# Kernel tuning notes

Hardware: AMD Instinct MI355X
Metric: run time of the kernel (lower is better)

The kernel has to match this reference:

```python
import jax, jax.numpy as jnp
import numpy as np

IN, H, L = 512, 1024, 2
N, T = 64, 256


def setup_inputs() -> dict:
    key = jax.random.key(0)
    ks = jax.random.split(key, 1 + 4 * L)
    x = jax.random.normal(ks[0], (N, T, IN), dtype=jnp.float32)
    inp = {"x": x}
    for l in range(L):
        d_in = IN if l == 0 else H
        s_x = 1.0 / np.sqrt(d_in)
        s_h = 1.0 / np.sqrt(H)
        # concatenated gate order: [i, f, g, o]
        inp[f"Wx{l}"] = jax.random.normal(ks[1 + 4 * l], (4 * H, d_in), dtype=jnp.float32) * s_x
        inp[f"Wh{l}"] = jax.random.normal(ks[2 + 4 * l], (4 * H, H), dtype=jnp.float32) * s_h
        inp[f"b{l}"] = jax.random.normal(ks[3 + 4 * l], (4 * H,), dtype=jnp.float32) * 0.1
        # peephole weights for [i, f, o] (original inits these to zero; randomized here)
        inp[f"Wc{l}"] = jax.random.normal(ks[4 + 4 * l], (3, H), dtype=jnp.float32) * 0.1
    return inp


def _lstm_forward(x, params):
    # params: list of (Wx [4H,d_in], Wh [4H,H], b [4H], Wc [3,H]) per layer
    n = x.shape[0]
    h0 = jnp.zeros((L, n, H), dtype=x.dtype)
    c0 = jnp.zeros((L, n, H), dtype=x.dtype)

    def step(carry, x_t):
        hs, cs = carry
        new_h, new_c = [], []
        inp_t = x_t
        for l, (Wx, Wh, b, Wc) in enumerate(params):
            h, c = hs[l], cs[l]
            gates = inp_t @ Wx.T + h @ Wh.T + b  # [n, 4H]
            gi, gf, gg, go = jnp.split(gates, 4, axis=-1)
            i = jax.nn.sigmoid(gi + Wc[0] * c)
            f = jax.nn.sigmoid(gf + Wc[1] * c)  # computed but unused (faithful to source)
            g = jnp.tanh(gg)
            o = jax.nn.sigmoid(go + Wc[2] * c)
            ct = g * c + i * g          # faithful: forget gate not applied
            ht = o * jnp.tanh(c)        # faithful: uses OLD cell state
            new_h.append(ht)
            new_c.append(ct)
            inp_t = ht  # dropout p=0 -> identity
        hs = jnp.stack(new_h)
        cs = jnp.stack(new_c)
        return (hs, cs), new_h[-1]

    (hs, cs), outs = jax.lax.scan(step, (h0, c0), jnp.swapaxes(x, 0, 1))
    out = jnp.swapaxes(outs, 0, 1)  # [N, T, H]
    return out, (hs[-1], cs[-1])


def reference(x, Wx0, Wh0, b0, Wc0, Wx1, Wh1, b1, Wc1):
    params = [(Wx0, Wh0, b0, Wc0), (Wx1, Wh1, b1, Wc1)]
    return _lstm_forward(x, params)
```

## Files before the change

### kernel.cpp

```cpp
#include <hip/hip_runtime.h>
#include <stdint.h>


#define T_STEPS 256
#define HDIM    1024
#define NB      64
#define INDIM   512
#define NWG     256
#define TPB     256
#define PRING   8

typedef _Float16 f16;
typedef __attribute__((ext_vector_type(8))) _Float16 f16x8;
typedef __attribute__((ext_vector_type(4))) float    f32x4;

#define CNT_OFF 0
#define XB_OFF  81920
#define H0_OFF  16859136
#define H1_OFF  50544640
#define C0_OFF  84230144
#define C1_OFF  84492288
#define P0_OFF  84754432
#define P1_OFF  91045888

__device__ __forceinline__ float sigm(float x)     { return 1.0f / (1.0f + __expf(-x)); }
__device__ __forceinline__ float tanhfast(float x) { float e = __expf(2.0f * x); return 1.0f - 2.0f / (e + 1.0f); }

__device__ __forceinline__ void arrive(int* c) {
  __hip_atomic_fetch_add(c, 1, __ATOMIC_RELAXED, __HIP_MEMORY_SCOPE_AGENT);
}
__device__ __forceinline__ void wait_ge(int* c, int v) {
  while (__hip_atomic_load(c, __ATOMIC_RELAXED, __HIP_MEMORY_SCOPE_AGENT) < v)
    __builtin_amdgcn_s_sleep(1);
  __atomic_signal_fence(__ATOMIC_ACQUIRE);
}
__device__ __forceinline__ void wait_flag(int* f, int tgt) {
  while (__hip_atomic_load(f, __ATOMIC_RELAXED, __HIP_MEMORY_SCOPE_AGENT) < tgt)
    __builtin_amdgcn_s_sleep(1);
}
__device__ __forceinline__ void sti(int* p, int v) {
  __hip_atomic_store(p, v, __ATOMIC_RELAXED, __HIP_MEMORY_SCOPE_AGENT);
}
__device__ __forceinline__ void st2h(f16* p, float a, float b) {
  union { f16 h[2]; uint32_t u; } cc; cc.h[0] = (f16)a; cc.h[1] = (f16)b;
  __hip_atomic_store((uint32_t*)p, cc.u, __ATOMIC_RELAXED, __HIP_MEMORY_SCOPE_AGENT);
}
__device__ __forceinline__ void st8a(void* p, unsigned long long v) {
  __hip_atomic_store((unsigned long long*)p, v, __ATOMIC_RELAXED, __HIP_MEMORY_SCOPE_AGENT);
}
__device__ __forceinline__ unsigned long long ld8(const float* p) {
  return __hip_atomic_load((const unsigned long long*)p, __ATOMIC_RELAXED, __HIP_MEMORY_SCOPE_AGENT);
}

template<int K>
__device__ __forceinline__ void gemm48_lds(const f16* __restrict__ Aw,
                                           const f16* wl, int lr, int wv, int quad,
                                           f32x4 (&acc)[4][3]) {
  constexpr int NIT = K / 128;
  const f16* a0 = Aw + (size_t)(lr +  0) * K;
  const f16* a1 = Aw + (size_t)(lr + 16) * K;
  const f16* a2 = Aw + (size_t)(lr + 32) * K;
  const f16* a3 = Aw + (size_t)(lr + 48) * K;
  f16x8 A0[NIT], A1[NIT], A2[NIT], A3[NIT];
#pragma unroll
  for (int it = 0; it < NIT; ++it) {
    const int kk = it * 32;
    A0[it] = *(const f16x8*)(a0 + kk);
    A1[it] = *(const f16x8*)(a1 + kk);
    A2[it] = *(const f16x8*)(a2 + kk);
    A3[it] = *(const f16x8*)(a3 + kk);
  }
  const f16* b0r = wl + (size_t)(lr +  0) * K;
  const f16* b1r = wl + (size_t)(lr + 16) * K;
  const f16* b2r = wl + (size_t)(lr + 32) * K;
  const int s  = lr & 7;
  const int cb = wv * (K / 32);
#pragma unroll
  for (int it = 0; it < NIT; ++it) {
    const int ch = ((cb + it * 4 + quad) ^ s) << 3;
    f16x8 B0 = *(const f16x8*)(b0r + ch);
    f16x8 B1 = *(const f16x8*)(b1r + ch);
    f16x8 B2 = *(const f16x8*)(b2r + ch);
    acc[0][0] = __builtin_amdgcn_mfma_f32_16x16x32_f16(A0[it], B0, acc[0][0], 0, 0, 0);
    acc[0][1] = __builtin_amdgcn_mfma_f32_16x16x32_f16(A0[it], B1, acc[0][1], 0, 0, 0);
    acc[0][2] = __builtin_amdgcn_mfma_f32_16x16x32_f16(A0[it], B2, acc[0][2], 0, 0, 0);
    acc[1][0] = __builtin_amdgcn_mfma_f32_16x16x32_f16(A1[it], B0, acc[1][0], 0, 0, 0);
    acc[1][1] = __builtin_amdgcn_mfma_f32_16x16x32_f16(A1[it], B1, acc[1][1], 0, 0, 0);
    acc[1][2] = __builtin_amdgcn_mfma_f32_16x16x32_f16(A1[it], B2, acc[1][2], 0, 0, 0);
    acc[2][0] = __builtin_amdgcn_mfma_f32_16x16x32_f16(A2[it], B0, acc[2][0], 0, 0, 0);
    acc[2][1] = __builtin_amdgcn_mfma_f32_16x16x32_f16(A2[it], B1, acc[2][1], 0, 0, 0);
    acc[2][2] = __builtin_amdgcn_mfma_f32_16x16x32_f16(A2[it], B2, acc[2][2], 0, 0, 0);
    acc[3][0] = __builtin_amdgcn_mfma_f32_16x16x32_f16(A3[it], B0, acc[3][0], 0, 0, 0);
    acc[3][1] = __builtin_amdgcn_mfma_f32_16x16x32_f16(A3[it], B1, acc[3][1], 0, 0, 0);
    acc[3][2] = __builtin_amdgcn_mfma_f32_16x16x32_f16(A3[it], B2, acc[3][2], 0, 0, 0);
  }
}

__global__ __launch_bounds__(TPB, 1) void lstm_pers(
    const float* __restrict__ x,
    const float* __restrict__ Wx0, const float* __restrict__ Wh0,
    const float* __restrict__ b0,  const float* __restrict__ Wc0,
    const float* __restrict__ Wx1, const float* __restrict__ Wh1,
    const float* __restrict__ b1,  const float* __restrict__ Wc1,
    float* __restrict__ out, char* __restrict__ ws)
{
  int* cbase = (int*)(ws + CNT_OFF);
  int* proCnt = cbase;
  auto FLG = [&](int g, int i) { return cbase + 16 + ((g * 64 + i) << 4); };

  f16* XB   = (f16*)(ws + XB_OFF);
  f16* H0   = (f16*)(ws + H0_OFF);
  f16* H1   = (f16*)(ws + H1_OFF);
  float* C0 = (float*)(ws + C0_OFF);
  float* C1 = (float*)(ws + C1_OFF);
  float* P0b = (float*)(ws + P0_OFF);
  float* P1b = (float*)(ws + P1_OFF);

  __shared__ float lds[4][64][52];
  __shared__ f16 wlds[48 * 1024];

  const int tid  = threadIdx.x;
  const int wg   = blockIdx.x;
  const int gtid = wg * TPB + tid;
  const int GSZ  = NWG * TPB;

  const int grp  = wg >> 6;
  const int ug   = wg & 63;
  const int lane = tid & 63;
  const int wv   = tid >> 6;
  const int quad = lane >> 4;
  const int lr   = lane & 15;

  const float* Wsrc; int K;
  switch (grp) {
    case 0:  Wsrc = Wx0; K = 512;  break;
    case 1:  Wsrc = Wh0; K = 1024; break;
    case 2:  Wsrc = Wx1; K = 1024; break;
    default: Wsrc = Wh1; K = 1024; break;
  }
  const int Kq = K >> 2;

  {
    const int rsh = (K == 512) ? 6 : 7;
    const int cpr = 1 << rsh;
    for (int c = tid; c < 48 * cpr; c += TPB) {
      const int row = c >> rsh, ch = c & (cpr - 1);
      const int gate = row >> 4, j = row & 15;
      const int R = ug * 16 + j + (gate == 1 ? 2048 : (gate == 2 ? 3072 : 0));
      const float* src = Wsrc + (size_t)R * K + (ch << 3);
      f32x4 f0 = *(const f32x4*)src;
      f32x4 f1 = *(const f32x4*)(src + 4);
      f16x8 h8;
      h8[0]=(f16)f0[0]; h8[1]=(f16)f0[1]; h8[2]=(f16)f0[2]; h8[3]=(f16)f0[3];
      h8[4]=(f16)f1[0]; h8[5]=(f16)f1[1]; h8[6]=(f16)f1[2]; h8[7]=(f16)f1[3];
      const int chs = ch ^ (row & 7);
      *(f16x8*)(wlds + (size_t)row * K + (chs << 3)) = h8;
    }
  }
  for (int idx = gtid; idx < T_STEPS * NB * 256; idx += GSZ) {
    int t = idx >> 14, n = (idx >> 8) & 63, i2 = (idx & 255) << 1;
    const float* src = x + (size_t)n * (T_STEPS * INDIM) + (size_t)t * INDIM + i2;
    st2h(&XB[(size_t)idx << 1], src[0], src[1]);
  }

  __builtin_amdgcn_s_waitcnt(0);
  __syncthreads();
  if (tid == 0) { arrive(proCnt); wait_ge(proCnt, NWG); }
  __syncthreads();

  const float* bb = (grp == 1) ? b0 : b1;
  const float* wc = (grp == 1) ? Wc0 : Wc1;
  float* cst = (grp == 1) ? C0 : C1;

  const int m_e = tid >> 2, j0 = (tid & 3) << 2;

  for (int t = 0; t < T_STEPS; ++t) {
    if (tid < 64) {
      if (grp == 0)      { if (t >= PRING) wait_flag(FLG(1, tid), t - PRING + 1); }
      else if (grp == 1) { wait_flag(FLG(0, tid), t + 1); if (t) wait_flag(FLG(1, tid), t); }
      else if (grp == 2) { wait_flag(FLG(1, tid), t + 1); if (t >= PRING) wait_flag(FLG(3, tid), t - PRING + 1); }
      else               { wait_flag(FLG(2, tid), t + 1); if (t) wait_flag(FLG(3, tid), t); }
    }
    __atomic_signal_fence(__ATOMIC_ACQUIRE);
    __syncthreads();

    const f16* Abase;
    if (grp == 0)      Abase = XB + (size_t)t * NB * INDIM;
    else if (grp == 1) Abase = H0 + (size_t)t * NB * HDIM;
    else if (grp == 2) Abase = H0 + (size_t)(t + 1) * NB * HDIM;
    else               Abase = H1 + (size_t)t * NB * HDIM;

    unsigned long long pr0, pr1, pr2, pr3, pr4, pr5;
    if (grp & 1) {
      const float* Pb = (grp == 1 ? P0b : P1b) + (size_t)(t & (PRING - 1)) * NB * 3072;
      const float* pbase = Pb + (size_t)m_e * 3072 + ug * 48 + j0;
      pr0 = ld8(pbase);      pr1 = ld8(pbase + 2);
      pr2 = ld8(pbase + 16); pr3 = ld8(pbase + 18);
      pr4 = ld8(pbase + 32); pr5 = ld8(pbase + 34);
    }

    f32x4 acc[4][3];
#pragma unroll
    for (int mt = 0; mt < 4; ++mt)
#pragma unroll
      for (int nt = 0; nt < 3; ++nt)
        acc[mt][nt] = (f32x4){0.f, 0.f, 0.f, 0.f};

    const f16* Aw = Abase + wv * Kq + quad * 8;
    if (grp == 0) gemm48_lds<512>(Aw, wlds, lr, wv, quad, acc);
    else          gemm48_lds<1024>(Aw, wlds, lr, wv, quad, acc);

#pragma unroll
    for (int mt = 0; mt < 4; ++mt)
#pragma unroll
      for (int nt = 0; nt < 3; ++nt)
#pragma unroll
        for (int r = 0; r < 4; ++r)
          lds[wv][mt * 16 + quad * 4 + r][nt * 16 + lr] = acc[mt][nt][r];
    __syncthreads();

    if ((grp & 1) == 0) {
      float* Pb = (grp == 0 ? P0b : P1b) + (size_t)(t & (PRING - 1)) * NB * 3072;
#pragma unroll
      for (int r = 0; r < 6; ++r) {
        const int s  = r * 256 + tid;
        const int m  = s / 24, cp = s - m * 24;
        const int c0 = cp << 1;
        float v0 = lds[0][m][c0]     + lds[1][m][c0]     + lds[2][m][c0]     + lds[3][m][c0];
        float v1 = lds[0][m][c0 + 1] + lds[1][m][c0 + 1] + lds[2][m][c0 + 1] + lds[3][m][c0 + 1];
        union { float f[2]; unsigned long long u; } pp; pp.f[0] = v0; pp.f[1] = v1;
        st8a(Pb + (size_t)m * 3072 + ug * 48 + c0, pp.u);
      }
    } else {
      union { unsigned long long u; float f[2]; } q0, q1, q2, q3, q4, q5;
      q0.u = pr0; q1.u = pr1; q2.u = pr2; q3.u = pr3; q4.u = pr4; q5.u = pr5;
      f32x4 vi = (f32x4){0.f, 0.f, 0.f, 0.f};
      f32x4 vg = vi, vo = vi;
#pragma unroll
      for (int w = 0; w < 4; ++w) {
        vi += *(const f32x4*)&lds[w][m_e][j0];
        vg += *(const f32x4*)&lds[w][m_e][16 + j0];
        vo += *(const f32x4*)&lds[w][m_e][32 + j0];
      }
      const float pif[4] = {q0.f[0], q0.f[1], q1.f[0], q1.f[1]};
      const float pgf[4] = {q2.f[0], q2.f[1], q3.f[0], q3.f[1]};
      const float pof[4] = {q4.f[0], q4.f[1], q5.f[0], q5.f[1]};
      f16* Hdst = (grp == 1 ? H0 : H1) + (size_t)(t + 1) * NB * HDIM;
      const int u0 = ug * 16 + j0;
      float* crow = cst + (size_t)m_e * HDIM + u0;
      f32x4 c4  = *(const f32x4*)crow;
      f32x4 b_i = *(const f32x4*)(bb + u0);
      f32x4 b_g = *(const f32x4*)(bb + 2048 + u0);
      f32x4 b_o = *(const f32x4*)(bb + 3072 + u0);
      f32x4 wci = *(const f32x4*)(wc + u0);
      f32x4 wco = *(const f32x4*)(wc + 2048 + u0);
      f32x4 hv, cn;
#pragma unroll
      for (int k = 0; k < 4; ++k) {
        float gi = vi[k] + pif[k] + b_i[k];
        float gg = vg[k] + pgf[k] + b_g[k];
        float go = vo[k] + pof[k] + b_o[k];
        float cold = c4[k];
        float iv = sigm(gi + wci[k] * cold);
        float gv = tanhfast(gg);
        float ov = sigm(go + wco[k] * cold);
        cn[k] = gv * (cold + iv);
        hv[k] = ov * tanhfast(cold);
      }
      *(f32x4*)crow = cn;
      union { f16 h[4]; unsigned long long u; } hh;
      hh.h[0]=(f16)hv[0]; hh.h[1]=(f16)hv[1]; hh.h[2]=(f16)hv[2]; hh.h[3]=(f16)hv[3];
      st8a(&Hdst[(size_t)m_e * HDIM + u0], hh.u);
      if (grp == 3) {
        *(f32x4*)&out[(size_t)m_e * (T_STEPS * HDIM) + (size_t)t * HDIM + u0] = hv;
        if (t == T_STEPS - 1) {
          *(f32x4*)&out[(size_t)NB * T_STEPS * HDIM + (size_t)m_e * HDIM + u0] = hv;
          *(f32x4*)&out[(size_t)NB * T_STEPS * HDIM + NB * HDIM + (size_t)m_e * HDIM + u0] = cn;
        }
      }
    }

    __builtin_amdgcn_s_waitcnt(0);
    __syncthreads();
    if (tid == 0) sti(FLG(grp, ug), t + 1);
  }
}

extern "C" void kernel_launch(void* const* d_in, const int* in_sizes, int n_in,
                              void* d_out, int out_size, void* d_ws, size_t ws_size,
                              hipStream_t stream) {
  const float* x   = (const float*)d_in[0];
  const float* Wx0 = (const float*)d_in[1];
  const float* Wh0 = (const float*)d_in[2];
  const float* b0  = (const float*)d_in[3];
  const float* Wc0 = (const float*)d_in[4];
  const float* Wx1 = (const float*)d_in[5];
  const float* Wh1 = (const float*)d_in[6];
  const float* b1  = (const float*)d_in[7];
  const float* Wc1 = (const float*)d_in[8];
  char* ws = (char*)d_ws;

  hipMemsetAsync(ws + CNT_OFF, 0, 81920, stream);
  hipMemsetAsync(ws + H0_OFF, 0, NB * HDIM * 2, stream);
  hipMemsetAsync(ws + H1_OFF, 0, NB * HDIM * 2, stream);
  hipMemsetAsync(ws + C0_OFF, 0, 2 * NB * HDIM * 4, stream);

  hipLaunchKernelGGL(lstm_pers, dim3(NWG), dim3(TPB), 0, stream,
                     x, Wx0, Wh0, b0, Wc0, Wx1, Wh1, b1, Wc1,
                     (float*)d_out, ws);
}
```

Before: 2.259 ms.

## Per-wave flag waits, packed flags, hoisted bias loads, output stores after signal

Replaces the step-start barrier, where 64 threads polled every flag before a block-wide __syncthreads, with per-wave waits. Each wave polls only the producer flags covering the 16 units whose rows it consumes, so it can start its GEMM as soon as its own inputs are ready. Flags are packed contiguously instead of padded 64 bytes apart. Bias and peephole weights are loaded once before the time loop, the cell-state load is issued early, and the global output store is moved after the flag publish so it stays off the critical path. The risks are flag false sharing, and whether dropping the barrier keeps correct visibility across waves, for example of the P buffer data.

```diff
diff --git a/kernel.cpp b/kernel.cpp
--- a/kernel.cpp
+++ b/kernel.cpp
@@ -33,10 +33,6 @@
   while (__hip_atomic_load(c, __ATOMIC_RELAXED, __HIP_MEMORY_SCOPE_AGENT) < v)
     __builtin_amdgcn_s_sleep(1);
   __atomic_signal_fence(__ATOMIC_ACQUIRE);
-}
-__device__ __forceinline__ void wait_flag(int* f, int tgt) {
-  while (__hip_atomic_load(f, __ATOMIC_RELAXED, __HIP_MEMORY_SCOPE_AGENT) < tgt)
-    __builtin_amdgcn_s_sleep(1);
 }
 __device__ __forceinline__ void sti(int* p, int v) {
   __hip_atomic_store(p, v, __ATOMIC_RELAXED, __HIP_MEMORY_SCOPE_AGENT);
@@ -106,7 +102,7 @@
 {
   int* cbase = (int*)(ws + CNT_OFF);
   int* proCnt = cbase;
-  auto FLG = [&](int g, int i) { return cbase + 16 + ((g * 64 + i) << 4); };
+  auto FLG = [&](int g, int i) { return cbase + 16 + g * 64 + i; };
 
   f16* XB   = (f16*)(ws + XB_OFF);
   f16* H0   = (f16*)(ws + H0_OFF);
@@ -168,21 +164,43 @@
   if (tid == 0) { arrive(proCnt); wait_ge(proCnt, NWG); }
   __syncthreads();
 
-  const float* bb = (grp == 1) ? b0 : b1;
-  const float* wc = (grp == 1) ? Wc0 : Wc1;
   float* cst = (grp == 1) ? C0 : C1;
-
   const int m_e = tid >> 2, j0 = (tid & 3) << 2;
+  const int u0  = ug * 16 + j0;
+  float* crow = cst + (size_t)m_e * HDIM + u0;
+
+  f32x4 b_i{}, b_g{}, b_o{}, wci{}, wco{};
+  if (grp & 1) {
+    const float* bb = (grp == 1) ? b0 : b1;
+    const float* wc = (grp == 1) ? Wc0 : Wc1;
+    b_i = *(const f32x4*)(bb + u0);
+    b_g = *(const f32x4*)(bb + 2048 + u0);
+    b_o = *(const f32x4*)(bb + 3072 + u0);
+    wci = *(const f32x4*)(wc + u0);
+    wco = *(const f32x4*)(wc + 2048 + u0);
+  }
 
   for (int t = 0; t < T_STEPS; ++t) {
-    if (tid < 64) {
-      if (grp == 0)      { if (t >= PRING) wait_flag(FLG(1, tid), t - PRING + 1); }
-      else if (grp == 1) { wait_flag(FLG(0, tid), t + 1); if (t) wait_flag(FLG(1, tid), t); }
-      else if (grp == 2) { wait_flag(FLG(1, tid), t + 1); if (t >= PRING) wait_flag(FLG(3, tid), t - PRING + 1); }
-      else               { wait_flag(FLG(2, tid), t + 1); if (t) wait_flag(FLG(3, tid), t); }
-    }
-    __atomic_signal_fence(__ATOMIC_ACQUIRE);
-    __syncthreads();
+    {
+      int* myp = nullptr; int tgt = 0;
+      if (grp == 0) {
+        if (lane == 0 && t >= PRING) { myp = FLG(1, ug); tgt = t - PRING + 1; }
+      } else if (grp == 1) {
+        if (lane < 16 && t > 0)      { myp = FLG(1, wv * 16 + lr); tgt = t; }
+        else if (lane == 16)         { myp = FLG(0, ug); tgt = t + 1; }
+      } else if (grp == 2) {
+        if (lane < 16)               { myp = FLG(1, wv * 16 + lr); tgt = t + 1; }
+        else if (lane == 16 && t >= PRING) { myp = FLG(3, ug); tgt = t - PRING + 1; }
+      } else {
+        if (lane < 16 && t > 0)      { myp = FLG(3, wv * 16 + lr); tgt = t; }
+        else if (lane == 16)         { myp = FLG(2, ug); tgt = t + 1; }
+      }
+      if (myp) {
+        while (__hip_atomic_load(myp, __ATOMIC_RELAXED, __HIP_MEMORY_SCOPE_AGENT) < tgt)
+          __builtin_amdgcn_s_sleep(1);
+      }
+      __atomic_signal_fence(__ATOMIC_ACQUIRE);
+    }
 
     const f16* Abase;
     if (grp == 0)      Abase = XB + (size_t)t * NB * INDIM;
@@ -191,12 +209,14 @@
     else               Abase = H1 + (size_t)t * NB * HDIM;
 
     unsigned long long pr0, pr1, pr2, pr3, pr4, pr5;
+    f32x4 c4{};
     if (grp & 1) {
       const float* Pb = (grp == 1 ? P0b : P1b) + (size_t)(t & (PRING - 1)) * NB * 3072;
       const float* pbase = Pb + (size_t)m_e * 3072 + ug * 48 + j0;
       pr0 = ld8(pbase);      pr1 = ld8(pbase + 2);
       pr2 = ld8(pbase + 16); pr3 = ld8(pbase + 18);
       pr4 = ld8(pbase + 32); pr5 = ld8(pbase + 34);
+      c4 = *(const f32x4*)crow;
     }
 
     f32x4 acc[4][3];
@@ -219,6 +239,7 @@
           lds[wv][mt * 16 + quad * 4 + r][nt * 16 + lr] = acc[mt][nt][r];
     __syncthreads();
 
+    f32x4 hv, cn;
     if ((grp & 1) == 0) {
       float* Pb = (grp == 0 ? P0b : P1b) + (size_t)(t & (PRING - 1)) * NB * 3072;
 #pragma unroll
@@ -246,15 +267,6 @@
       const float pgf[4] = {q2.f[0], q2.f[1], q3.f[0], q3.f[1]};
       const float pof[4] = {q4.f[0], q4.f[1], q5.f[0], q5.f[1]};
       f16* Hdst = (grp == 1 ? H0 : H1) + (size_t)(t + 1) * NB * HDIM;
-      const int u0 = ug * 16 + j0;
-      float* crow = cst + (size_t)m_e * HDIM + u0;
-      f32x4 c4  = *(const f32x4*)crow;
-      f32x4 b_i = *(const f32x4*)(bb + u0);
-      f32x4 b_g = *(const f32x4*)(bb + 2048 + u0);
-      f32x4 b_o = *(const f32x4*)(bb + 3072 + u0);
-      f32x4 wci = *(const f32x4*)(wc + u0);
-      f32x4 wco = *(const f32x4*)(wc + 2048 + u0);
-      f32x4 hv, cn;
 #pragma unroll
       for (int k = 0; k < 4; ++k) {
         float gi = vi[k] + pif[k] + b_i[k];
@@ -271,18 +283,19 @@
       union { f16 h[4]; unsigned long long u; } hh;
       hh.h[0]=(f16)hv[0]; hh.h[1]=(f16)hv[1]; hh.h[2]=(f16)hv[2]; hh.h[3]=(f16)hv[3];
       st8a(&Hdst[(size_t)m_e * HDIM + u0], hh.u);
-      if (grp == 3) {
-        *(f32x4*)&out[(size_t)m_e * (T_STEPS * HDIM) + (size_t)t * HDIM + u0] = hv;
-        if (t == T_STEPS - 1) {
-          *(f32x4*)&out[(size_t)NB * T_STEPS * HDIM + (size_t)m_e * HDIM + u0] = hv;
-          *(f32x4*)&out[(size_t)NB * T_STEPS * HDIM + NB * HDIM + (size_t)m_e * HDIM + u0] = cn;
-        }
-      }
     }
 
     __builtin_amdgcn_s_waitcnt(0);
     __syncthreads();
     if (tid == 0) sti(FLG(grp, ug), t + 1);
+
+    if (grp == 3) {
+      *(f32x4*)&out[(size_t)m_e * (T_STEPS * HDIM) + (size_t)t * HDIM + u0] = hv;
+      if (t == T_STEPS - 1) {
+        *(f32x4*)&out[(size_t)NB * T_STEPS * HDIM + (size_t)m_e * HDIM + u0] = hv;
+        *(f32x4*)&out[(size_t)NB * T_STEPS * HDIM + NB * HDIM + (size_t)m_e * HDIM + u0] = cn;
+      }
+    }
   }
 }
 
```

Measured after the change: 2.673 ms. 18.3% more time.
